# Performance work log

Measured on AMD Instinct MI355X. Metric: run time of the kernel, lower is better.

Reference implementation:

```python
import jax, jax.numpy as jnp
import numpy as np

B, S, E, H = 2, 2048, 768, 12
D = E // H  # head_dim = 64
SCALE = D ** -0.5
NEG = float(np.finfo(np.float32).max)


def setup_inputs() -> dict:
    key = jax.random.key(0)
    ks = jax.random.split(key, 6)
    std = E ** -0.5
    return {
        "inputs": jax.random.normal(ks[0], (B, S, E), dtype=jnp.float32),
        "mask": jax.random.randint(ks[1], (B, S), 0, 2, dtype=jnp.int32),
        "w_qkv": jax.random.normal(ks[2], (3 * E, E), dtype=jnp.float32) * std,
        "b_qkv": jax.random.normal(ks[3], (3 * E,), dtype=jnp.float32) * 0.01,
        "w_proj": jax.random.normal(ks[4], (E, E), dtype=jnp.float32) * std,
        "b_proj": jax.random.normal(ks[5], (E,), dtype=jnp.float32) * 0.01,
    }


def reference(inputs, mask, w_qkv, b_qkv, w_proj, b_proj):
    # qkv projection: (B,S,E) -> (B,S,3E) -> (3,B,H,S,D)
    qkv = (jnp.einsum("bse,fe->bsf", inputs, w_qkv) + b_qkv)
    qkv = qkv.reshape(B, S, 3, H, D).transpose(2, 0, 3, 1, 4)
    q, k, v = qkv[0], qkv[1], qkv[2]
    # scaled dot-product scores (B,H,S,S)
    qk = jnp.einsum("bhqd,bhkd->bhqk", q, k) * SCALE
    # mask (B,S) broadcasts over key axis, matching torch broadcasting
    qk = qk + mask.astype(jnp.float32)[:, None, None, :] * (-NEG)
    attn = jax.nn.softmax(qk, axis=-1)
    x = jnp.einsum("bhqk,bhkd->bhqd", attn, v)  # (B,H,S,D)
    x = x.transpose(0, 2, 1, 3).reshape(B, S, E)
    # dropouts are identity in eval mode
    return jnp.einsum("bse,fe->bsf", x, w_proj) + b_proj
```

## Files before the change

kernel.cpp:

```cpp
#include <hip/hip_runtime.h>
#include <stdint.h>

#define S_LEN 2048
#define EMB   768
#define NHEAD 12
#define HDIM  64

typedef __attribute__((ext_vector_type(8)))  __bf16       bf16x8;
typedef __attribute__((ext_vector_type(4)))  float        f32x4;
typedef __attribute__((ext_vector_type(16))) float        f32x16;
typedef __attribute__((ext_vector_type(2)))  unsigned int u32x2;
typedef __attribute__((ext_vector_type(4)))  unsigned int u32x4;

__device__ __forceinline__ uint16_t f32_to_bf16(float f) {
  uint32_t u = __float_as_uint(f);
  u += 0x7FFFu + ((u >> 16) & 1u);
  return (uint16_t)(u >> 16);
}

__device__ __forceinline__ uint32_t cvtpk_bf16(float lo, float hi) {
  uint32_t r;
  asm("v_cvt_pk_bf16_f32 %0, %1, %2" : "=v"(r) : "v"(lo), "v"(hi));
  return r;
}

#if __has_builtin(__builtin_amdgcn_exp2f)
#define EXP2F(x) __builtin_amdgcn_exp2f(x)
#else
#define EXP2F(x) exp2f(x)
#endif

#define ZERO16 {0.f,0.f,0.f,0.f,0.f,0.f,0.f,0.f,0.f,0.f,0.f,0.f,0.f,0.f,0.f,0.f}

__device__ __forceinline__ int swz64(int idx) {
  return idx ^ (((idx >> 6) & 7) << 3);
}

__device__ __forceinline__ void gload16(uint16_t* lds, const uint16_t* g) {
  __builtin_amdgcn_global_load_lds((const __attribute__((address_space(1))) void*)g,
                                   (__attribute__((address_space(3))) void*)lds, 16, 0, 0);
}

__global__ __launch_bounds__(256) void cvt_all(const float4* __restrict__ i0, ushort4* __restrict__ o0, int n0,
                                               const float4* __restrict__ i1, ushort4* __restrict__ o1, int n1,
                                               const float4* __restrict__ i2, ushort4* __restrict__ o2, int n2) {
  int gid = blockIdx.x * blockDim.x + threadIdx.x;
  const float4* src;
  ushort4* dst;
  int idx;
  if (gid < n0)           { src = i0; dst = o0; idx = gid; }
  else if (gid < n0 + n1) { src = i1; dst = o1; idx = gid - n0; }
  else if (gid < n0 + n1 + n2) { src = i2; dst = o2; idx = gid - n0 - n1; }
  else return;
  float4 v = src[idx];
  ushort4 o;
  o.x = f32_to_bf16(v.x); o.y = f32_to_bf16(v.y);
  o.z = f32_to_bf16(v.z); o.w = f32_to_bf16(v.w);
  dst[idx] = o;
}

__global__ __launch_bounds__(256) void qkv_gemm(const uint16_t* __restrict__ A,
                                                const uint16_t* __restrict__ W,
                                                const float* __restrict__ bias,
                                                uint16_t* __restrict__ qb,
                                                uint16_t* __restrict__ kb,
                                                uint16_t* __restrict__ vb) {
  __shared__ __align__(16) uint16_t As[128 * 64];
  __shared__ __align__(16) uint16_t Bs[64 * 64];
  const int t    = threadIdx.x;
  const int lane = t & 63;
  const int wv   = t >> 6;
  const int wr   = wv >> 1, wc = wv & 1;
  const int wg   = (blockIdx.x & 7) * 144 + (blockIdx.x >> 3);
  const int bm   = wg & 31;
  const int bn   = wg >> 5;

  const uint16_t* Ag = A + (size_t)bm * 128 * 768;
  const uint16_t* Wg = W + (size_t)bn * 64 * 768;

  f32x4 zf = {0.f, 0.f, 0.f, 0.f};
  f32x4 acc[4][2];
#pragma unroll
  for (int m = 0; m < 4; m++)
#pragma unroll
    for (int n = 0; n < 2; n++) acc[m][n] = zf;

  for (int k0 = 0; k0 < 768; k0 += 64) {
#pragma unroll
    for (int j = 0; j < 4; j++) {
      int p = j * 256 + t;
      int r = p >> 3, x = p & 7;
      int scol = (x ^ (r & 7)) << 3;
      gload16(&As[p * 8], Ag + (size_t)r * 768 + k0 + scol);
    }
#pragma unroll
    for (int j = 0; j < 2; j++) {
      int p = j * 256 + t;
      int r = p >> 3, x = p & 7;
      int scol = (x ^ (r & 7)) << 3;
      gload16(&Bs[p * 8], Wg + (size_t)r * 768 + k0 + scol);
    }
    __syncthreads();
#pragma unroll
    for (int kk = 0; kk < 2; kk++) {
      const int kc = kk * 32 + (lane >> 4) * 8;
      bf16x8 af[4], bf[2];
#pragma unroll
      for (int m = 0; m < 4; m++)
        af[m] = *reinterpret_cast<const bf16x8*>(&As[swz64((wr * 64 + m * 16 + (lane & 15)) * 64 + kc)]);
#pragma unroll
      for (int n = 0; n < 2; n++)
        bf[n] = *reinterpret_cast<const bf16x8*>(&Bs[swz64((wc * 32 + n * 16 + (lane & 15)) * 64 + kc)]);
#pragma unroll
      for (int m = 0; m < 4; m++)
#pragma unroll
        for (int n = 0; n < 2; n++)
          acc[m][n] = __builtin_amdgcn_mfma_f32_16x16x32_bf16(af[m], bf[n], acc[m][n], 0, 0, 0);
    }
    __syncthreads();
  }

#pragma unroll
  for (int n = 0; n < 2; n++) {
    const int f = bn * 64 + wc * 32 + n * 16 + (lane & 15);
    const float bv  = bias[f];
    const int  c    = f / 768;
    const int  rem  = f % 768;
    const int  h    = rem >> 6, d = rem & 63;
    const float scl = (c == 0) ? 0.125f * 1.44269504f : 1.0f;
#pragma unroll
    for (int m = 0; m < 4; m++) {
#pragma unroll
      for (int r = 0; r < 4; r++) {
        int i = bm * 128 + wr * 64 + m * 16 + (lane >> 4) * 4 + r;
        int b = i >> 11, s = i & 2047;
        uint16_t val = f32_to_bf16((acc[m][n][r] + bv) * scl);
        if (c == 0)
          qb[(((size_t)b * NHEAD + h) * S_LEN + s) * HDIM + d] = val;
        else if (c == 1)
          kb[(((size_t)b * NHEAD + h) * S_LEN + s) * HDIM + d] = val;
        else
          vb[(((size_t)b * NHEAD + h) * HDIM + d) * S_LEN + s] = val;
      }
    }
  }
}

__global__ __launch_bounds__(256, 3) void attn_kernel(const uint16_t* __restrict__ Q,
                                                      const uint16_t* __restrict__ Kb,
                                                      const uint16_t* __restrict__ Vb,
                                                      const int* __restrict__ mask,
                                                      uint16_t* __restrict__ X) {
  __shared__ __align__(16) uint16_t Kd[2][64 * 64];
  __shared__ __align__(16) uint16_t Vd[2][64 * 64];
  __shared__ __align__(16) float    mb_s[S_LEN];
  __shared__ float Lc[2][32];

  const int t    = threadIdx.x;
  const int lane = t & 63;
  const int hl   = lane >> 5;
  const int q31  = lane & 31;
  const int wv   = t >> 6;
  const int qg   = wv & 1;
  const int kh   = wv >> 1;
  const int wg   = (blockIdx.x & 7) * 96 + (blockIdx.x >> 3);
  const int qblk = wg & 31;
  const int bh   = wg >> 5;
  const int b    = bh / NHEAD, hd = bh % NHEAD;

  const uint16_t* Qh = Q  + (size_t)bh * S_LEN * HDIM;
  const uint16_t* Kh = Kb + (size_t)bh * S_LEN * HDIM;
  const uint16_t* Vh = Vb + (size_t)bh * HDIM * S_LEN;
  const int q0 = qblk * 64 + qg * 32;

  {
    int4 m0 = *reinterpret_cast<const int4*>(&mask[b * S_LEN + t * 8]);
    int4 m1 = *reinterpret_cast<const int4*>(&mask[b * S_LEN + t * 8 + 4]);
    float4 f0, f1;
    f0.x = m0.x ? -1e30f : 0.0f; f0.y = m0.y ? -1e30f : 0.0f;
    f0.z = m0.z ? -1e30f : 0.0f; f0.w = m0.w ? -1e30f : 0.0f;
    f1.x = m1.x ? -1e30f : 0.0f; f1.y = m1.y ? -1e30f : 0.0f;
    f1.z = m1.z ? -1e30f : 0.0f; f1.w = m1.w ? -1e30f : 0.0f;
    *reinterpret_cast<float4*>(&mb_s[t * 8])     = f0;
    *reinterpret_cast<float4*>(&mb_s[t * 8 + 4]) = f1;
  }

  bf16x8 qf[4];
#pragma unroll
  for (int s = 0; s < 4; s++)
    qf[s] = *reinterpret_cast<const bf16x8*>(Qh + (size_t)(q0 + q31) * HDIM + 16 * s + 8 * hl);

  f32x16 oacc[2] = {ZERO16, ZERO16};
  float lsum = 0.f;

  const uint16_t* kga[2]; const uint16_t* vga[2]; int lof[2];
#pragma unroll
  for (int j = 0; j < 2; j++) {
    int p = j * 256 + t, r = p >> 3, x = p & 7;
    int scol = (x ^ (r & 7)) << 3;
    kga[j] = Kh + (size_t)r * HDIM + scol;
    vga[j] = Vh + (size_t)r * S_LEN + scol;
    lof[j] = p * 8;
  }
  auto stage = [&](int nb, int it2) {
#pragma unroll
    for (int j = 0; j < 2; j++) {
      gload16(&Kd[nb][lof[j]], kga[j] + it2 * 64 * HDIM);
      gload16(&Vd[nb][lof[j]], vga[j] + it2 * 64);
    }
  };

  stage(0, 0);
  __syncthreads();

#pragma unroll 2
  for (int it = 0; it < 32; ++it) {
    const int cur = it & 1;
    __builtin_amdgcn_s_barrier();
    __builtin_amdgcn_sched_barrier(0);
    if (it + 1 < 32) {
      stage(cur ^ 1, it + 1);
      asm volatile("s_waitcnt vmcnt(4)" ::: "memory");
    } else {
      asm volatile("s_waitcnt vmcnt(0)" ::: "memory");
    }
    __builtin_amdgcn_s_barrier();
    __builtin_amdgcn_sched_barrier(0);

    f32x16 scc = ZERO16;
    __builtin_amdgcn_s_setprio(1);
#pragma unroll
    for (int s = 0; s < 4; s++) {
      bf16x8 kf = *reinterpret_cast<const bf16x8*>(&Kd[cur][swz64((kh * 32 + q31) * 64 + 16 * s + 8 * hl)]);
      scc = __builtin_amdgcn_mfma_f32_32x32x16_bf16(kf, qf[s], scc, 0, 0, 0);
    }
    __builtin_amdgcn_s_setprio(0);

    uint32_t w[4][2];
#pragma unroll
    for (int s2 = 0; s2 < 4; s2++) {
      f32x4 mbv = *reinterpret_cast<const f32x4*>(&mb_s[it * 64 + kh * 32 + s2 * 8 + hl * 4]);
      float p0 = EXP2F(scc[4 * s2 + 0] + mbv[0]);
      float p1 = EXP2F(scc[4 * s2 + 1] + mbv[1]);
      float p2 = EXP2F(scc[4 * s2 + 2] + mbv[2]);
      float p3 = EXP2F(scc[4 * s2 + 3] + mbv[3]);
      lsum += (p0 + p1) + (p2 + p3);
      w[s2][0] = cvtpk_bf16(p0, p1);
      w[s2][1] = cvtpk_bf16(p2, p3);
    }

    bf16x8 pb[2];
#pragma unroll
    for (int ks = 0; ks < 2; ks++) {
      u32x2 r0 = __builtin_amdgcn_permlane32_swap(w[2 * ks][0], w[2 * ks + 1][0], false, false);
      u32x2 r1 = __builtin_amdgcn_permlane32_swap(w[2 * ks][1], w[2 * ks + 1][1], false, false);
      u32x4 uu;
      uu.x = r0.x; uu.y = r1.x; uu.z = r0.y; uu.w = r1.y;
      pb[ks] = __builtin_bit_cast(bf16x8, uu);
    }

    __builtin_amdgcn_s_setprio(1);
#pragma unroll
    for (int mt = 0; mt < 2; mt++)
#pragma unroll
      for (int ks = 0; ks < 2; ks++) {
        bf16x8 vf = *reinterpret_cast<const bf16x8*>(&Vd[cur][swz64((mt * 32 + q31) * 64 + kh * 32 + ks * 16 + hl * 8)]);
        oacc[mt] = __builtin_amdgcn_mfma_f32_32x32x16_bf16(vf, pb[ks], oacc[mt], 0, 0, 0);
      }
    __builtin_amdgcn_s_setprio(0);
  }

  lsum += __shfl_xor(lsum, 32);

  float* Oc = qg ? (float*)&Vd[0][0] : (float*)&Kd[0][0];
  if (kh == 1) {
#pragma unroll
    for (int mt = 0; mt < 2; mt++)
#pragma unroll
      for (int e = 0; e < 16; e++) {
        int d = mt * 32 + (e & 3) + (e >> 2) * 8 + hl * 4;
        Oc[d * 32 + q31] = oacc[mt][e];
      }
    if (hl == 0) Lc[qg][q31] = lsum;
  }
  __syncthreads();
  if (kh == 0) {
    float linv = 1.0f / (lsum + Lc[qg][q31]);
    uint16_t* Xr = X + ((size_t)b * S_LEN + q0 + q31) * EMB + hd * HDIM;
#pragma unroll
    for (int mt = 0; mt < 2; mt++)
#pragma unroll
      for (int s2 = 0; s2 < 4; s2++) {
        int d0 = mt * 32 + s2 * 8 + hl * 4;
        float v0 = (oacc[mt][4 * s2 + 0] + Oc[(d0 + 0) * 32 + q31]) * linv;
        float v1 = (oacc[mt][4 * s2 + 1] + Oc[(d0 + 1) * 32 + q31]) * linv;
        float v2 = (oacc[mt][4 * s2 + 2] + Oc[(d0 + 2) * 32 + q31]) * linv;
        float v3 = (oacc[mt][4 * s2 + 3] + Oc[(d0 + 3) * 32 + q31]) * linv;
        uint2 ww;
        ww.x = cvtpk_bf16(v0, v1);
        ww.y = cvtpk_bf16(v2, v3);
        *reinterpret_cast<uint2*>(Xr + d0) = ww;
      }
  }
}

__global__ __launch_bounds__(256) void proj_gemm(const uint16_t* __restrict__ A,
                                                 const uint16_t* __restrict__ W,
                                                 const float* __restrict__ bias,
                                                 float* __restrict__ out) {
  __shared__ __align__(16) uint16_t As[64 * 64];
  __shared__ __align__(16) uint16_t Bs[64 * 64];
  const int t    = threadIdx.x;
  const int lane = t & 63;
  const int wv   = t >> 6;
  const int wr   = wv >> 1, wc = wv & 1;
  const int bm   = blockIdx.x & 63;
  const int bn   = blockIdx.x >> 6;

  const uint16_t* Ag = A + (size_t)bm * 64 * 768;
  const uint16_t* Wg = W + (size_t)bn * 64 * 768;

  f32x4 zf = {0.f, 0.f, 0.f, 0.f};
  f32x4 acc[2][2];
#pragma unroll
  for (int m = 0; m < 2; m++)
#pragma unroll
    for (int n = 0; n < 2; n++) acc[m][n] = zf;

  for (int k0 = 0; k0 < 768; k0 += 64) {
#pragma unroll
    for (int j = 0; j < 2; j++) {
      int p = j * 256 + t;
      int r = p >> 3, x = p & 7;
      int scol = (x ^ (r & 7)) << 3;
      gload16(&As[p * 8], Ag + (size_t)r * 768 + k0 + scol);
      gload16(&Bs[p * 8], Wg + (size_t)r * 768 + k0 + scol);
    }
    __syncthreads();
#pragma unroll
    for (int kk = 0; kk < 2; kk++) {
      const int kc = kk * 32 + (lane >> 4) * 8;
      bf16x8 af[2], bf[2];
#pragma unroll
      for (int m = 0; m < 2; m++)
        af[m] = *reinterpret_cast<const bf16x8*>(&As[swz64((wr * 32 + m * 16 + (lane & 15)) * 64 + kc)]);
#pragma unroll
      for (int n = 0; n < 2; n++)
        bf[n] = *reinterpret_cast<const bf16x8*>(&Bs[swz64((wc * 32 + n * 16 + (lane & 15)) * 64 + kc)]);
#pragma unroll
      for (int m = 0; m < 2; m++)
#pragma unroll
        for (int n = 0; n < 2; n++)
          acc[m][n] = __builtin_amdgcn_mfma_f32_16x16x32_bf16(af[m], bf[n], acc[m][n], 0, 0, 0);
    }
    __syncthreads();
  }

#pragma unroll
  for (int n = 0; n < 2; n++) {
    const int f = bn * 64 + wc * 32 + n * 16 + (lane & 15);
    const float bv = bias[f];
#pragma unroll
    for (int m = 0; m < 2; m++)
#pragma unroll
      for (int r = 0; r < 4; r++) {
        int i = bm * 64 + wr * 32 + m * 16 + (lane >> 4) * 4 + r;
        out[(size_t)i * 768 + f] = acc[m][n][r] + bv;
      }
  }
}

extern "C" void kernel_launch(void* const* d_in, const int* in_sizes, int n_in,
                              void* d_out, int out_size, void* d_ws, size_t ws_size,
                              hipStream_t stream) {
  const float* inputs = (const float*)d_in[0];
  const int*   mask   = (const int*)d_in[1];
  const float* w_qkv  = (const float*)d_in[2];
  const float* b_qkv  = (const float*)d_in[3];
  const float* w_proj = (const float*)d_in[4];
  const float* b_proj = (const float*)d_in[5];
  float* out = (float*)d_out;

  uint16_t* a_bf  = (uint16_t*)d_ws;
  uint16_t* wq_bf = a_bf  + (size_t)4096 * 768;
  uint16_t* wp_bf = wq_bf + (size_t)2304 * 768;
  uint16_t* q_bf  = wp_bf + (size_t)768 * 768;
  uint16_t* k_bf  = q_bf  + (size_t)24 * 2048 * 64;
  uint16_t* v_bf  = k_bf  + (size_t)24 * 2048 * 64;
  uint16_t* x_bf  = v_bf  + (size_t)24 * 2048 * 64;

  const int n0 = 4096 * 768 / 4, n1 = 2304 * 768 / 4, n2 = 768 * 768 / 4;
  cvt_all<<<(n0 + n1 + n2 + 255) / 256, 256, 0, stream>>>(
      (const float4*)inputs, (ushort4*)a_bf, n0,
      (const float4*)w_qkv,  (ushort4*)wq_bf, n1,
      (const float4*)w_proj, (ushort4*)wp_bf, n2);
  qkv_gemm<<<32 * 36, 256, 0, stream>>>(a_bf, wq_bf, b_qkv, q_bf, k_bf, v_bf);
  attn_kernel<<<24 * 32, 256, 0, stream>>>(q_bf, k_bf, v_bf, mask, x_bf);
  proj_gemm<<<64 * 12, 256, 0, stream>>>(x_bf, wp_bf, b_proj, out);
}
```

Before: 99.58 us.

## Fuse fp32-to-bf16 conversion into GEMM tile loads, drop separate cvt kernel

Removes the standalone conversion kernel and has qkv_gemm and proj_gemm load fp32 inputs and weights directly, converting them to bf16 while storing into LDS. This saves one launch and the round trip of writing and rereading the bf16 copies. In exchange the GEMMs now read twice the bytes per tile and stage through registers instead of async global-to-LDS loads. Each block also repeats the conversion for data shared across blocks.

```diff
diff --git a/kernel.cpp b/kernel.cpp
--- a/kernel.cpp
+++ b/kernel.cpp
@@ -41,26 +41,19 @@
                                    (__attribute__((address_space(3))) void*)lds, 16, 0, 0);
 }
 
-__global__ __launch_bounds__(256) void cvt_all(const float4* __restrict__ i0, ushort4* __restrict__ o0, int n0,
-                                               const float4* __restrict__ i1, ushort4* __restrict__ o1, int n1,
-                                               const float4* __restrict__ i2, ushort4* __restrict__ o2, int n2) {
-  int gid = blockIdx.x * blockDim.x + threadIdx.x;
-  const float4* src;
-  ushort4* dst;
-  int idx;
-  if (gid < n0)           { src = i0; dst = o0; idx = gid; }
-  else if (gid < n0 + n1) { src = i1; dst = o1; idx = gid - n0; }
-  else if (gid < n0 + n1 + n2) { src = i2; dst = o2; idx = gid - n0 - n1; }
-  else return;
-  float4 v = src[idx];
-  ushort4 o;
-  o.x = f32_to_bf16(v.x); o.y = f32_to_bf16(v.y);
-  o.z = f32_to_bf16(v.z); o.w = f32_to_bf16(v.w);
-  dst[idx] = o;
-}
-
-__global__ __launch_bounds__(256) void qkv_gemm(const uint16_t* __restrict__ A,
-                                                const uint16_t* __restrict__ W,
+__device__ __forceinline__ void stage_cvt(uint16_t* lds_dst, const float* src) {
+  f32x4 f0 = *reinterpret_cast<const f32x4*>(src);
+  f32x4 f1 = *reinterpret_cast<const f32x4*>(src + 4);
+  u32x4 uu;
+  uu.x = cvtpk_bf16(f0[0], f0[1]);
+  uu.y = cvtpk_bf16(f0[2], f0[3]);
+  uu.z = cvtpk_bf16(f1[0], f1[1]);
+  uu.w = cvtpk_bf16(f1[2], f1[3]);
+  *reinterpret_cast<u32x4*>(lds_dst) = uu;
+}
+
+__global__ __launch_bounds__(256) void qkv_gemm(const float* __restrict__ A32,
+                                                const float* __restrict__ W32,
                                                 const float* __restrict__ bias,
                                                 uint16_t* __restrict__ qb,
                                                 uint16_t* __restrict__ kb,
@@ -75,8 +68,25 @@
   const int bm   = wg & 31;
   const int bn   = wg >> 5;
 
-  const uint16_t* Ag = A + (size_t)bm * 128 * 768;
-  const uint16_t* Wg = W + (size_t)bn * 64 * 768;
+  const float* Ag = A32 + (size_t)bm * 128 * 768;
+  const float* Wg = W32 + (size_t)bn * 64 * 768;
+
+  int aoff[4], lofA[4];
+#pragma unroll
+  for (int j = 0; j < 4; j++) {
+    int p = j * 256 + t, r = p >> 3, x = p & 7;
+    int scol = (x ^ (r & 7)) << 3;
+    aoff[j] = r * 768 + scol;
+    lofA[j] = p * 8;
+  }
+  int woff[2], lofB[2];
+#pragma unroll
+  for (int j = 0; j < 2; j++) {
+    int p = j * 256 + t, r = p >> 3, x = p & 7;
+    int scol = (x ^ (r & 7)) << 3;
+    woff[j] = r * 768 + scol;
+    lofB[j] = p * 8;
+  }
 
   f32x4 zf = {0.f, 0.f, 0.f, 0.f};
   f32x4 acc[4][2];
@@ -87,19 +97,11 @@
 
   for (int k0 = 0; k0 < 768; k0 += 64) {
 #pragma unroll
-    for (int j = 0; j < 4; j++) {
-      int p = j * 256 + t;
-      int r = p >> 3, x = p & 7;
-      int scol = (x ^ (r & 7)) << 3;
-      gload16(&As[p * 8], Ag + (size_t)r * 768 + k0 + scol);
-    }
-#pragma unroll
-    for (int j = 0; j < 2; j++) {
-      int p = j * 256 + t;
-      int r = p >> 3, x = p & 7;
-      int scol = (x ^ (r & 7)) << 3;
-      gload16(&Bs[p * 8], Wg + (size_t)r * 768 + k0 + scol);
-    }
+    for (int j = 0; j < 4; j++)
+      stage_cvt(&As[lofA[j]], Ag + aoff[j] + k0);
+#pragma unroll
+    for (int j = 0; j < 2; j++)
+      stage_cvt(&Bs[lofB[j]], Wg + woff[j] + k0);
     __syncthreads();
 #pragma unroll
     for (int kk = 0; kk < 2; kk++) {
@@ -305,7 +307,7 @@
 }
 
 __global__ __launch_bounds__(256) void proj_gemm(const uint16_t* __restrict__ A,
-                                                 const uint16_t* __restrict__ W,
+                                                 const float* __restrict__ W32,
                                                  const float* __restrict__ bias,
                                                  float* __restrict__ out) {
   __shared__ __align__(16) uint16_t As[64 * 64];
@@ -317,8 +319,8 @@
   const int bm   = blockIdx.x & 63;
   const int bn   = blockIdx.x >> 6;
 
-  const uint16_t* Ag = A + (size_t)bm * 64 * 768;
-  const uint16_t* Wg = W + (size_t)bn * 64 * 768;
+  const uint16_t* Ag = A   + (size_t)bm * 64 * 768;
+  const float*    Wg = W32 + (size_t)bn * 64 * 768;
 
   f32x4 zf = {0.f, 0.f, 0.f, 0.f};
   f32x4 acc[2][2];
@@ -334,7 +336,7 @@
       int r = p >> 3, x = p & 7;
       int scol = (x ^ (r & 7)) << 3;
       gload16(&As[p * 8], Ag + (size_t)r * 768 + k0 + scol);
-      gload16(&Bs[p * 8], Wg + (size_t)r * 768 + k0 + scol);
+      stage_cvt(&Bs[p * 8], Wg + (size_t)r * 768 + k0 + scol);
     }
     __syncthreads();
 #pragma unroll
@@ -381,20 +383,12 @@
   const float* b_proj = (const float*)d_in[5];
   float* out = (float*)d_out;
 
-  uint16_t* a_bf  = (uint16_t*)d_ws;
-  uint16_t* wq_bf = a_bf  + (size_t)4096 * 768;
-  uint16_t* wp_bf = wq_bf + (size_t)2304 * 768;
-  uint16_t* q_bf  = wp_bf + (size_t)768 * 768;
+  uint16_t* q_bf  = (uint16_t*)d_ws;
   uint16_t* k_bf  = q_bf  + (size_t)24 * 2048 * 64;
   uint16_t* v_bf  = k_bf  + (size_t)24 * 2048 * 64;
   uint16_t* x_bf  = v_bf  + (size_t)24 * 2048 * 64;
 
-  const int n0 = 4096 * 768 / 4, n1 = 2304 * 768 / 4, n2 = 768 * 768 / 4;
-  cvt_all<<<(n0 + n1 + n2 + 255) / 256, 256, 0, stream>>>(
-      (const float4*)inputs, (ushort4*)a_bf, n0,
-      (const float4*)w_qkv,  (ushort4*)wq_bf, n1,
-      (const float4*)w_proj, (ushort4*)wp_bf, n2);
-  qkv_gemm<<<32 * 36, 256, 0, stream>>>(a_bf, wq_bf, b_qkv, q_bf, k_bf, v_bf);
+  qkv_gemm<<<32 * 36, 256, 0, stream>>>(inputs, w_qkv, b_qkv, q_bf, k_bf, v_bf);
   attn_kernel<<<24 * 32, 256, 0, stream>>>(q_bf, k_bf, v_bf, mask, x_bf);
-  proj_gemm<<<64 * 12, 256, 0, stream>>>(x_bf, wp_bf, b_proj, out);
-}
+  proj_gemm<<<64 * 12, 256, 0, stream>>>(x_bf, w_proj, b_proj, out);
+}
```

Result: slower. 117.2 us (+17.7%).

## Compact unmasked keys/values and loop attention only over valid key tiles

Applied to the files above, without the earlier changes.

Adds a mask_scan kernel that prefix-sums the key mask per batch, builds compacted key positions and a padded tile count, and zero-fills the padding rows. The QKV GEMM scatters K and V into compacted positions and drops masked keys, so the attention loop runs only over the non-masked key tiles. With a random half-masked input this roughly halves the attention work. The cost is an extra small launch, a scattered epilogue, and an added barrier before the output reduction. Because masked keys get exactly zero softmax weight in the reference, the result stays valid for any mask, except when every key in a batch row is masked.

```diff
diff --git a/kernel.cpp b/kernel.cpp
--- a/kernel.cpp
+++ b/kernel.cpp
@@ -59,9 +59,58 @@
   dst[idx] = o;
 }
 
+__global__ __launch_bounds__(256) void mask_scan(const int* __restrict__ mask,
+                                                 int* __restrict__ cpos,
+                                                 float* __restrict__ mbc,
+                                                 int* __restrict__ ntp,
+                                                 uint16_t* __restrict__ kb,
+                                                 uint16_t* __restrict__ vb) {
+  const int b = blockIdx.x;
+  const int t = threadIdx.x;
+  __shared__ int part[257];
+  int m[8], u = 0;
+#pragma unroll
+  for (int j = 0; j < 8; j++) {
+    m[j] = mask[b * S_LEN + t * 8 + j];
+    u += (m[j] == 0);
+  }
+  part[t] = u;
+  __syncthreads();
+  if (t == 0) {
+    int run = 0;
+    for (int i = 0; i < 256; i++) { int v = part[i]; part[i] = run; run += v; }
+    part[256] = run;
+  }
+  __syncthreads();
+  const int nb = part[256];
+  int base = part[t];
+#pragma unroll
+  for (int j = 0; j < 8; j++) {
+    int sc = (m[j] == 0) ? base : -1;
+    if (m[j] == 0) base++;
+    cpos[b * S_LEN + t * 8 + j] = sc;
+    mbc[b * S_LEN + t * 8 + j] = ((t * 8 + j) < nb) ? 0.0f : -1e30f;
+  }
+  const int padN = (nb + 63) & ~63;
+  if (t == 0) ntp[b] = padN >> 6;
+  const int npad = padN - nb;
+  if (npad > 0) {
+    const int tot = npad * NHEAD * HDIM;
+    for (int idx = t; idx < tot; idx += 256) {
+      int d   = idx & (HDIM - 1);
+      int rem = idx >> 6;
+      int row = rem % npad;
+      int h   = rem / npad;
+      kb[(((size_t)b * NHEAD + h) * S_LEN + nb + row) * HDIM + d] = 0;
+      vb[(((size_t)b * NHEAD + h) * HDIM + d) * S_LEN + nb + row] = 0;
+    }
+  }
+}
+
 __global__ __launch_bounds__(256) void qkv_gemm(const uint16_t* __restrict__ A,
                                                 const uint16_t* __restrict__ W,
                                                 const float* __restrict__ bias,
+                                                const int* __restrict__ cpos,
                                                 uint16_t* __restrict__ qb,
                                                 uint16_t* __restrict__ kb,
                                                 uint16_t* __restrict__ vb) {
@@ -135,12 +184,17 @@
         int i = bm * 128 + wr * 64 + m * 16 + (lane >> 4) * 4 + r;
         int b = i >> 11, s = i & 2047;
         uint16_t val = f32_to_bf16((acc[m][n][r] + bv) * scl);
-        if (c == 0)
+        if (c == 0) {
           qb[(((size_t)b * NHEAD + h) * S_LEN + s) * HDIM + d] = val;
-        else if (c == 1)
-          kb[(((size_t)b * NHEAD + h) * S_LEN + s) * HDIM + d] = val;
-        else
-          vb[(((size_t)b * NHEAD + h) * HDIM + d) * S_LEN + s] = val;
+        } else {
+          int sc = cpos[b * S_LEN + s];
+          if (sc >= 0) {
+            if (c == 1)
+              kb[(((size_t)b * NHEAD + h) * S_LEN + sc) * HDIM + d] = val;
+            else
+              vb[(((size_t)b * NHEAD + h) * HDIM + d) * S_LEN + sc] = val;
+          }
+        }
       }
     }
   }
@@ -149,7 +203,8 @@
 __global__ __launch_bounds__(256, 3) void attn_kernel(const uint16_t* __restrict__ Q,
                                                       const uint16_t* __restrict__ Kb,
                                                       const uint16_t* __restrict__ Vb,
-                                                      const int* __restrict__ mask,
+                                                      const float* __restrict__ mbc,
+                                                      const int* __restrict__ ntp,
                                                       uint16_t* __restrict__ X) {
   __shared__ __align__(16) uint16_t Kd[2][64 * 64];
   __shared__ __align__(16) uint16_t Vd[2][64 * 64];
@@ -172,15 +227,11 @@
   const uint16_t* Kh = Kb + (size_t)bh * S_LEN * HDIM;
   const uint16_t* Vh = Vb + (size_t)bh * HDIM * S_LEN;
   const int q0 = qblk * 64 + qg * 32;
+  const int nt = ntp[b];
 
   {
-    int4 m0 = *reinterpret_cast<const int4*>(&mask[b * S_LEN + t * 8]);
-    int4 m1 = *reinterpret_cast<const int4*>(&mask[b * S_LEN + t * 8 + 4]);
-    float4 f0, f1;
-    f0.x = m0.x ? -1e30f : 0.0f; f0.y = m0.y ? -1e30f : 0.0f;
-    f0.z = m0.z ? -1e30f : 0.0f; f0.w = m0.w ? -1e30f : 0.0f;
-    f1.x = m1.x ? -1e30f : 0.0f; f1.y = m1.y ? -1e30f : 0.0f;
-    f1.z = m1.z ? -1e30f : 0.0f; f1.w = m1.w ? -1e30f : 0.0f;
+    float4 f0 = *reinterpret_cast<const float4*>(&mbc[b * S_LEN + t * 8]);
+    float4 f1 = *reinterpret_cast<const float4*>(&mbc[b * S_LEN + t * 8 + 4]);
     *reinterpret_cast<float4*>(&mb_s[t * 8])     = f0;
     *reinterpret_cast<float4*>(&mb_s[t * 8 + 4]) = f1;
   }
@@ -202,11 +253,11 @@
     vga[j] = Vh + (size_t)r * S_LEN + scol;
     lof[j] = p * 8;
   }
-  auto stage = [&](int nb, int it2) {
+  auto stage = [&](int nb2, int it2) {
 #pragma unroll
     for (int j = 0; j < 2; j++) {
-      gload16(&Kd[nb][lof[j]], kga[j] + it2 * 64 * HDIM);
-      gload16(&Vd[nb][lof[j]], vga[j] + it2 * 64);
+      gload16(&Kd[nb2][lof[j]], kga[j] + it2 * 64 * HDIM);
+      gload16(&Vd[nb2][lof[j]], vga[j] + it2 * 64);
     }
   };
 
@@ -214,11 +265,11 @@
   __syncthreads();
 
 #pragma unroll 2
-  for (int it = 0; it < 32; ++it) {
+  for (int it = 0; it < nt; ++it) {
     const int cur = it & 1;
     __builtin_amdgcn_s_barrier();
     __builtin_amdgcn_sched_barrier(0);
-    if (it + 1 < 32) {
+    if (it + 1 < nt) {
       stage(cur ^ 1, it + 1);
       asm volatile("s_waitcnt vmcnt(4)" ::: "memory");
     } else {
@@ -271,6 +322,8 @@
   }
 
   lsum += __shfl_xor(lsum, 32);
+
+  __syncthreads();
 
   float* Oc = qg ? (float*)&Vd[0][0] : (float*)&Kd[0][0];
   if (kh == 1) {
@@ -388,13 +441,17 @@
   uint16_t* k_bf  = q_bf  + (size_t)24 * 2048 * 64;
   uint16_t* v_bf  = k_bf  + (size_t)24 * 2048 * 64;
   uint16_t* x_bf  = v_bf  + (size_t)24 * 2048 * 64;
+  int*      cpos  = (int*)(x_bf + (size_t)4096 * 768);
+  float*    mbc   = (float*)(cpos + 2 * 2048);
+  int*      ntp   = (int*)(mbc + 2 * 2048);
 
   const int n0 = 4096 * 768 / 4, n1 = 2304 * 768 / 4, n2 = 768 * 768 / 4;
   cvt_all<<<(n0 + n1 + n2 + 255) / 256, 256, 0, stream>>>(
       (const float4*)inputs, (ushort4*)a_bf, n0,
       (const float4*)w_qkv,  (ushort4*)wq_bf, n1,
       (const float4*)w_proj, (ushort4*)wp_bf, n2);
-  qkv_gemm<<<32 * 36, 256, 0, stream>>>(a_bf, wq_bf, b_qkv, q_bf, k_bf, v_bf);
-  attn_kernel<<<24 * 32, 256, 0, stream>>>(q_bf, k_bf, v_bf, mask, x_bf);
+  mask_scan<<<2, 256, 0, stream>>>(mask, cpos, mbc, ntp, k_bf, v_bf);
+  qkv_gemm<<<32 * 36, 256, 0, stream>>>(a_bf, wq_bf, b_qkv, cpos, q_bf, k_bf, v_bf);
+  attn_kernel<<<24 * 32, 256, 0, stream>>>(q_bf, k_bf, v_bf, mbc, ntp, x_bf);
   proj_gemm<<<64 * 12, 256, 0, stream>>>(x_bf, wp_bf, b_proj, out);
 }
```

Measured after the change: 108.2 us. 8.6% more time.
